# Performance work log

Measured on AMD Instinct MI355X. Metric: run time of the kernel, lower is better.

Reference implementation:

```python
import jax, jax.numpy as jnp
import numpy as np

N = 50000      # nodes
E = 800000     # edges
IN = 128       # in_channels
HID = 32       # hidden_channels per head
HEADS = 4
OUT = 16       # out_channels
NEG_SLOPE_ATT = 0.2   # GATv2Conv default negative_slope
NEG_SLOPE_ACT = 0.01  # F.leaky_relu default
EPS = 1e-16


def setup_inputs() -> dict:
    key = jax.random.key(0)
    ks = jax.random.split(key, 13)
    d1 = HEADS * HID  # 128
    g = lambda k, shape, fan: jax.random.normal(k, shape, jnp.float32) * (1.0 / np.sqrt(fan))
    return {
        "x": jax.random.normal(ks[0], (N, IN), jnp.float32),
        "edge_index": jax.random.randint(ks[1], (2, E), 0, N, dtype=jnp.int32),
        "edge_weight": jax.random.uniform(ks[2], (E,), jnp.float32),
        # conv1 (GATv2): lin_l, lin_r, att, bias
        "Wl1": g(ks[3], (IN, d1), IN), "Wr1": g(ks[4], (IN, d1), IN),
        "att1": g(ks[5], (HEADS, HID), HID), "b1": jnp.zeros((d1,), jnp.float32),
        # conv2
        "Wl2": g(ks[6], (d1, d1), d1), "Wr2": g(ks[7], (d1, d1), d1),
        "att2": g(ks[8], (HEADS, HID), HID), "b2": jnp.zeros((d1,), jnp.float32),
        # classifier
        "Wc": g(ks[9], (d1, OUT), d1), "bc": jnp.zeros((OUT,), jnp.float32),
    }


def gatv2_layer(x, Wl, Wr, att, bias, src, dst):
    n = x.shape[0]
    xl = (x @ Wl).reshape(n, HEADS, HID)  # source transform
    xr = (x @ Wr).reshape(n, HEADS, HID)  # target transform
    m = xl[src] + xr[dst]                                    # [Etot, H, C]
    e = jnp.sum(jax.nn.leaky_relu(m, NEG_SLOPE_ATT) * att, axis=-1)  # [Etot, H]
    # segment softmax over incoming edges of each target node
    emax = jax.ops.segment_max(e, dst, num_segments=n)       # [N, H]
    ex = jnp.exp(e - emax[dst])
    denom = jax.ops.segment_sum(ex, dst, num_segments=n)     # [N, H]
    alpha = ex / (denom[dst] + EPS)                          # [Etot, H]
    out = jax.ops.segment_sum(xl[src] * alpha[:, :, None], dst, num_segments=n)  # [N, H, C]
    return out.reshape(n, HEADS * HID) + bias


def reference(x, edge_index, edge_weight, Wl1, Wr1, att1, b1, Wl2, Wr2, att2, b2, Wc, bc):
    # GATv2Conv default add_self_loops=True
    loops = jnp.arange(N, dtype=edge_index.dtype)
    src = jnp.concatenate([edge_index[0], loops])
    dst = jnp.concatenate([edge_index[1], loops])
    h = gatv2_layer(x, Wl1, Wr1, att1, b1, src, dst)
    h = jax.nn.leaky_relu(h, NEG_SLOPE_ACT)
    h = gatv2_layer(h, Wl2, Wr2, att2, b2, src, dst)
    h = jax.nn.leaky_relu(h, NEG_SLOPE_ACT)
    logits = h @ Wc + bc
    return (logits, h)
```

## Files before the change

kernel.cpp:

```cpp
#include <hip/hip_runtime.h>
#include <hip/hip_fp16.h>


#define LOG2E 1.4426950408889634f
#define AST 40

typedef short bf16x8 __attribute__((ext_vector_type(8)));
typedef float f32x4 __attribute__((ext_vector_type(4)));

__device__ __forceinline__ unsigned short f2bf(float f) {
  union { float f; unsigned u; } x; x.f = f;
  unsigned r = x.u + 0x7fffu + ((x.u >> 16) & 1u);
  return (unsigned short)(r >> 16);
}
__device__ __forceinline__ float bf2f(unsigned short h) {
  union { unsigned u; float f; } x; x.u = ((unsigned)h) << 16;
  return x.f;
}
__device__ __forceinline__ void split4(float4 v, ushort4& h, ushort4& l) {
  h.x = f2bf(v.x); l.x = f2bf(v.x - bf2f(h.x));
  h.y = f2bf(v.y); l.y = f2bf(v.y - bf2f(h.y));
  h.z = f2bf(v.z); l.z = f2bf(v.z - bf2f(h.z));
  h.w = f2bf(v.w); l.w = f2bf(v.w - bf2f(h.w));
}

__device__ __forceinline__ float mixlo(float a, unsigned b, float c) {
  float d;
  asm("v_fma_mix_f32 %0, %1, %2, %3 op_sel_hi:[0,1,0]"
      : "=v"(d) : "v"(a), "v"(b), "v"(c));
  return d;
}
__device__ __forceinline__ float mixhi(float a, unsigned b, float c) {
  float d;
  asm("v_fma_mix_f32 %0, %1, %2, %3 op_sel:[0,1,0] op_sel_hi:[0,1,0]"
      : "=v"(d) : "v"(a), "v"(b), "v"(c));
  return d;
}
__device__ __forceinline__ float mixlo_abs(float a, unsigned b, float c) {
  float d;
  asm("v_fma_mix_f32 %0, %1, |%2|, %3 op_sel_hi:[0,1,0]"
      : "=v"(d) : "v"(a), "v"(b), "v"(c));
  return d;
}
__device__ __forceinline__ float mixhi_abs(float a, unsigned b, float c) {
  float d;
  asm("v_fma_mix_f32 %0, %1, |%2|, %3 op_sel:[0,1,0] op_sel_hi:[0,1,0]"
      : "=v"(d) : "v"(a), "v"(b), "v"(c));
  return d;
}
__device__ __forceinline__ unsigned pk_add(unsigned a, unsigned b) {
  union { unsigned u; __half2 h; } x, y, r;
  x.u = a; y.u = b;
  r.h = __hadd2(x.h, y.h);
  return r.u;
}


__global__ __launch_bounds__(256) void zero_i32(int* __restrict__ p, int n) {
  int i = blockIdx.x * 256 + threadIdx.x;
  if (i < n) p[i] = 0;
}

__global__ __launch_bounds__(256) void scan_blk(const int* __restrict__ cnt,
                                                int* __restrict__ excl,
                                                int* __restrict__ bsum, int n) {
  __shared__ int s[256];
  int t = threadIdx.x, i = blockIdx.x * 256 + t;
  int v = (i < n) ? (cnt[i] + 1) : 0;
  s[t] = v;
  __syncthreads();
#pragma unroll
  for (int off = 1; off < 256; off <<= 1) {
    int u = (t >= off) ? s[t - off] : 0;
    __syncthreads();
    s[t] += u;
    __syncthreads();
  }
  if (i < n) excl[i] = s[t] - v;
  if (t == 255) bsum[blockIdx.x] = s[255];
}

__global__ __launch_bounds__(256) void scan_bsum(int* __restrict__ bsum, int nb,
                                                 int* __restrict__ row_start, int n) {
  __shared__ int s[256];
  int t = threadIdx.x;
  int v = (t < nb) ? bsum[t] : 0;
  s[t] = v;
  __syncthreads();
#pragma unroll
  for (int off = 1; off < 256; off <<= 1) {
    int u = (t >= off) ? s[t - off] : 0;
    __syncthreads();
    s[t] += u;
    __syncthreads();
  }
  if (t < nb) bsum[t] = s[t] - v;
  if (t == 255) row_start[n] = s[255];
}

__global__ __launch_bounds__(256) void scan_add(int* __restrict__ row_start,
                                                const int* __restrict__ bsum,
                                                int* __restrict__ wpos,
                                                int* __restrict__ csr,
                                                int n, int padBase) {
  int i = blockIdx.x * 256 + threadIdx.x;
  if (i < n) {
    int r = row_start[i] + bsum[blockIdx.x];
    row_start[i] = r;
    wpos[i] = r + 1;
    csr[r] = i;
  }
  if (blockIdx.x == 0 && threadIdx.x < 16) csr[padBase + threadIdx.x] = 0;
}

__global__ __launch_bounds__(256) void convert_count(
    const float* __restrict__ Wl1, const float* __restrict__ Wr1,
    const float* __restrict__ Wl2, const float* __restrict__ Wr2,
    unsigned short* __restrict__ BT1h, unsigned short* __restrict__ BT1l,
    unsigned short* __restrict__ BT2h, unsigned short* __restrict__ BT2l,
    const int* __restrict__ dst, int* __restrict__ cnt, int E) {
  int b = blockIdx.x;
  if (b >= 256) {
    int i = (b - 256) * 256 + threadIdx.x;
    if (i < E) atomicAdd(&cnt[dst[i]], 1);
    return;
  }
  const float* Wl = (b < 128) ? Wl1 : Wl2;
  const float* Wr = (b < 128) ? Wr1 : Wr2;
  unsigned short* BTh = (b < 128) ? BT1h : BT2h;
  unsigned short* BTl = (b < 128) ? BT1l : BT2l;
  int idx = (b & 127) * 256 + threadIdx.x;
  int col = idx >> 7, k = idx & 127;
  float v = (col < 128) ? Wl[k * 128 + col] : Wr[k * 128 + (col - 128)];
  unsigned short h = f2bf(v);
  BTh[idx] = h;
  BTl[idx] = f2bf(v - bf2f(h));
}

enum { IN_F32 = 0, IN_BFPAIR = 1 };
template <int MODE, int FUSE>
__global__ __launch_bounds__(256) void gemm_mfma(
    const float* __restrict__ Af,
    const unsigned short* __restrict__ Ah, const unsigned short* __restrict__ Al,
    const unsigned short* __restrict__ BTh, const unsigned short* __restrict__ BTl,
    __half* __restrict__ Cl, __half* __restrict__ Cr, int nrows,
    const int* __restrict__ esrc, const int* __restrict__ edst,
    int* __restrict__ wpos, int* __restrict__ csr, int E, int sliceSize) {
  __shared__ __align__(16) unsigned short smem[4 * 128 * AST];
  int tid = threadIdx.x;
  int bx, by;
  if (FUSE) {
    int g = blockIdx.x / 9, r = blockIdx.x - g * 9;
    if (r < 5) {
      int sid = g * 5 + r;
      if (sid < 1024) {
        int per = (E + 1023) >> 10;
        int b0 = sid * per;
        int cnt = min(per, E - b0);
        if (cnt > 0) {
          int* ss = (int*)smem;
          int* sd = ss + per;
          for (int i = tid; i < cnt; i += 256) {
            ss[i] = esrc[b0 + i];
            sd[i] = edst[b0 + i];
          }
          __syncthreads();
          for (int sl = 0; sl < 8; ++sl) {
            int lo = sl * sliceSize, hi = lo + sliceSize;
            for (int i = tid; i < cnt; i += 256) {
              int d = sd[i];
              if (d >= lo && d < hi) {
                int p = atomicAdd(&wpos[d], 1);
                csr[p] = ss[i];
              }
            }
          }
        }
      }
      return;
    }
    int gid = g * 4 + (r - 5);
    int nbx = (nrows + 127) >> 7;
    if (gid >= nbx * 2) return;
    bx = gid >> 1;
    by = gid & 1;
  } else {
    bx = blockIdx.x;
    by = blockIdx.y;
  }

  unsigned short* sAh = smem;
  unsigned short* sAl = smem + 5120;
  unsigned short* sBh = smem + 10240;
  unsigned short* sBl = smem + 15360;

  int wave = tid >> 6, lane = tid & 63;
  int rowBase = bx * 128;
  int colBase = by * 128;
  int rowHalf = (wave >> 1) * 64;
  int colHalf = (wave & 1) * 64;
  int l15 = lane & 15, quad = lane >> 4;

  f32x4 acc[4][4];
#pragma unroll
  for (int m = 0; m < 4; ++m)
#pragma unroll
    for (int n = 0; n < 4; ++n) acc[m][n] = (f32x4){0.f, 0.f, 0.f, 0.f};

  for (int kc = 0; kc < 4; ++kc) {
#pragma unroll
    for (int i = 0; i < 2; ++i) {
      int idx = tid + i * 256;
      int row = idx >> 2, seg = idx & 3;
      int gr = rowBase + row;
      if (MODE == IN_F32) {
        float4 v0 = make_float4(0.f, 0.f, 0.f, 0.f), v1 = v0;
        if (gr < nrows) {
          v0 = *(const float4*)&Af[(size_t)gr * 128 + kc * 32 + seg * 8];
          v1 = *(const float4*)&Af[(size_t)gr * 128 + kc * 32 + seg * 8 + 4];
        }
        ushort4 h0, l0, h1, l1;
        split4(v0, h0, l0);
        split4(v1, h1, l1);
        *(ushort4*)&sAh[row * AST + seg * 8] = h0;
        *(ushort4*)&sAh[row * AST + seg * 8 + 4] = h1;
        *(ushort4*)&sAl[row * AST + seg * 8] = l0;
        *(ushort4*)&sAl[row * AST + seg * 8 + 4] = l1;
      } else {
        uint4 vh = make_uint4(0, 0, 0, 0), vl = vh;
        if (gr < nrows) {
          vh = *(const uint4*)&Ah[(size_t)gr * 128 + kc * 32 + seg * 8];
          vl = *(const uint4*)&Al[(size_t)gr * 128 + kc * 32 + seg * 8];
        }
        *(uint4*)&sAh[row * AST + seg * 8] = vh;
        *(uint4*)&sAl[row * AST + seg * 8] = vl;
      }
    }
#pragma unroll
    for (int i = 0; i < 2; ++i) {
      int idx = tid + i * 256;
      int col = idx >> 2, seg = idx & 3;
      *(uint4*)&sBh[col * AST + seg * 8] =
          *(const uint4*)&BTh[(size_t)(colBase + col) * 128 + kc * 32 + seg * 8];
      *(uint4*)&sBl[col * AST + seg * 8] =
          *(const uint4*)&BTl[(size_t)(colBase + col) * 128 + kc * 32 + seg * 8];
    }
    __syncthreads();

    bf16x8 afh[4], afl[4], bfh[4], bfl[4];
#pragma unroll
    for (int m = 0; m < 4; ++m) {
      int r = rowHalf + m * 16 + l15;
      afh[m] = *(const bf16x8*)&sAh[r * AST + quad * 8];
      afl[m] = *(const bf16x8*)&sAl[r * AST + quad * 8];
    }
#pragma unroll
    for (int n = 0; n < 4; ++n) {
      int cc = colHalf + n * 16 + l15;
      bfh[n] = *(const bf16x8*)&sBh[cc * AST + quad * 8];
      bfl[n] = *(const bf16x8*)&sBl[cc * AST + quad * 8];
    }
#pragma unroll
    for (int m = 0; m < 4; ++m)
#pragma unroll
      for (int n = 0; n < 4; ++n) {
        acc[m][n] = __builtin_amdgcn_mfma_f32_16x16x32_bf16(afh[m], bfh[n], acc[m][n], 0, 0, 0);
        acc[m][n] = __builtin_amdgcn_mfma_f32_16x16x32_bf16(afh[m], bfl[n], acc[m][n], 0, 0, 0);
        acc[m][n] = __builtin_amdgcn_mfma_f32_16x16x32_bf16(afl[m], bfh[n], acc[m][n], 0, 0, 0);
      }
    __syncthreads();
  }

  __half* __restrict__ C = (by == 0) ? Cl : Cr;
#pragma unroll
  for (int m = 0; m < 4; ++m)
#pragma unroll
    for (int r = 0; r < 4; ++r) {
      int grow = rowBase + rowHalf + m * 16 + quad * 4 + r;
      if (grow < nrows) {
#pragma unroll
        for (int n = 0; n < 4; ++n)
          C[(size_t)grow * 128 + colHalf + n * 16 + l15] = __float2half(acc[m][n][r]);
      }
    }
}

__global__ __launch_bounds__(256) void gat_attn(const __half* __restrict__ xl,
                                                const __half* __restrict__ xr,
                                                const int* __restrict__ row_start,
                                                const int* __restrict__ csr,
                                                const float* __restrict__ att,
                                                const float* __restrict__ bias,
                                                float* __restrict__ ofp,
                                                unsigned short* __restrict__ ohi,
                                                unsigned short* __restrict__ olo,
                                                int n_nodes) {
  int node = blockIdx.x * 4 + (threadIdx.x >> 6);
  if (node >= n_nodes) return;
  int lane = threadIdx.x & 63;
  int slot = lane >> 4;
  int l15 = lane & 15;
  int c0 = l15 * 8;

  unsigned hxr[4];
  {
    uint4 raw = *(const uint4*)&xr[(size_t)node * 128 + c0];
    const unsigned* q = (const unsigned*)&raw;
    hxr[0] = q[0]; hxr[1] = q[1]; hxr[2] = q[2]; hxr[3] = q[3];
  }
  float a06[8], a04[8];
  {
    float4 a0 = *(const float4*)&att[c0];
    float4 a1 = *(const float4*)&att[c0 + 4];
    float av[8] = {a0.x, a0.y, a0.z, a0.w, a1.x, a1.y, a1.z, a1.w};
    const float C06 = 0.6f * LOG2E, C04 = 0.4f * LOG2E;
#pragma unroll
    for (int k = 0; k < 8; ++k) { a06[k] = av[k] * C06; a04[k] = av[k] * C04; }
  }

  float acc[8];
#pragma unroll
  for (int k = 0; k < 8; ++k) acc[k] = 0.f;
  float lsum = 0.f;

#define EDGE_BODY(SRC, PVALID)                                                 \
  {                                                                            \
    uint4 raw = *(const uint4*)&xl[(size_t)(unsigned)(SRC)*128 + c0];          \
    const unsigned* xp = (const unsigned*)&raw;                                \
    float e0 = 0.f, e1 = 0.f;                                                  \
    _Pragma("unroll") for (int j = 0; j < 4; ++j) {                            \
      unsigned tw = pk_add(xp[j], hxr[j]);                                     \
      e0 = mixlo(a06[2 * j], tw, e0);                                          \
      e0 = mixlo_abs(a04[2 * j], tw, e0);                                      \
      e1 = mixhi(a06[2 * j + 1], tw, e1);                                      \
      e1 = mixhi_abs(a04[2 * j + 1], tw, e1);                                  \
    }                                                                          \
    float e = e0 + e1;                                                         \
    e += __shfl_xor(e, 1);                                                     \
    e += __shfl_xor(e, 2);                                                     \
    float p = (PVALID) ? __builtin_amdgcn_exp2f(e) : 0.f;                      \
    lsum += p;                                                                 \
    _Pragma("unroll") for (int j = 0; j < 4; ++j) {                            \
      acc[2 * j] = mixlo(p, xp[j], acc[2 * j]);                                \
      acc[2 * j + 1] = mixhi(p, xp[j], acc[2 * j + 1]);                        \
    }                                                                          \
  }

  int beg = row_start[node], end = row_start[node + 1];
  int deg = end - beg;
  int fullEnd = beg + (deg & ~15);

  for (int base = beg; base < fullEnd; base += 16) {
    int b0 = base + 4 * slot;
    int s0 = csr[b0], s1 = csr[b0 + 1], s2 = csr[b0 + 2], s3 = csr[b0 + 3];
    EDGE_BODY(s0, true);
    EDGE_BODY(s1, true);
    EDGE_BODY(s2, true);
    EDGE_BODY(s3, true);
  }
  for (int base = fullEnd; base < end; base += 4) {
    int idx = base + slot;
    int src = csr[idx];
    EDGE_BODY(src, idx < end);
  }
#undef EDGE_BODY

  lsum += __shfl_xor(lsum, 16);
  lsum += __shfl_xor(lsum, 32);
#pragma unroll
  for (int k = 0; k < 8; ++k) {
    acc[k] += __shfl_xor(acc[k], 16);
    acc[k] += __shfl_xor(acc[k], 32);
  }

  if (slot == 0) {
    float4 b0v = *(const float4*)&bias[c0];
    float4 b1v = *(const float4*)&bias[c0 + 4];
    float bv[8] = {b0v.x, b0v.y, b0v.z, b0v.w, b1v.x, b1v.y, b1v.z, b1v.w};
    float inv = 1.f / (lsum + 1e-16f);
    float o[8];
#pragma unroll
    for (int k = 0; k < 8; ++k) {
      float v = fmaf(acc[k], inv, bv[k]);
      o[k] = fmaf(0.495f, fabsf(v), 0.505f * v);
    }
    if (ofp) {
      *(float4*)&ofp[(size_t)node * 128 + c0] = make_float4(o[0], o[1], o[2], o[3]);
      *(float4*)&ofp[(size_t)node * 128 + c0 + 4] = make_float4(o[4], o[5], o[6], o[7]);
    }
    if (ohi) {
      ushort4 h0, h1, lo0, lo1;
      h0.x = f2bf(o[0]); lo0.x = f2bf(o[0] - bf2f(h0.x));
      h0.y = f2bf(o[1]); lo0.y = f2bf(o[1] - bf2f(h0.y));
      h0.z = f2bf(o[2]); lo0.z = f2bf(o[2] - bf2f(h0.z));
      h0.w = f2bf(o[3]); lo0.w = f2bf(o[3] - bf2f(h0.w));
      h1.x = f2bf(o[4]); lo1.x = f2bf(o[4] - bf2f(h1.x));
      h1.y = f2bf(o[5]); lo1.y = f2bf(o[5] - bf2f(h1.y));
      h1.z = f2bf(o[6]); lo1.z = f2bf(o[6] - bf2f(h1.z));
      h1.w = f2bf(o[7]); lo1.w = f2bf(o[7] - bf2f(h1.w));
      *(ushort4*)&ohi[(size_t)node * 128 + c0] = h0;
      *(ushort4*)&ohi[(size_t)node * 128 + c0 + 4] = h1;
      *(ushort4*)&olo[(size_t)node * 128 + c0] = lo0;
      *(ushort4*)&olo[(size_t)node * 128 + c0 + 4] = lo1;
    }
  }
}

__global__ __launch_bounds__(256) void classifier_kernel(const float4* __restrict__ h4,
                                                         const float* __restrict__ Wc,
                                                         const float* __restrict__ bc,
                                                         float* __restrict__ logits,
                                                         int n) {
  __shared__ float sW[2048];
  __shared__ float sb[16];
  int t = threadIdx.x;
#pragma unroll
  for (int i = 0; i < 8; ++i) sW[t + i * 256] = Wc[t + i * 256];
  if (t < 16) sb[t] = bc[t];
  __syncthreads();
  int node = blockIdx.x * 256 + t;
  if (node >= n) return;
  float acc[16];
#pragma unroll
  for (int o = 0; o < 16; ++o) acc[o] = sb[o];
  for (int c4 = 0; c4 < 32; ++c4) {
    float4 hv = h4[(unsigned)node * 32 + c4];
    const float* w = &sW[c4 * 64];
#pragma unroll
    for (int o = 0; o < 16; ++o) {
      acc[o] = fmaf(hv.x, w[o], acc[o]);
      acc[o] = fmaf(hv.y, w[16 + o], acc[o]);
      acc[o] = fmaf(hv.z, w[32 + o], acc[o]);
      acc[o] = fmaf(hv.w, w[48 + o], acc[o]);
    }
  }
#pragma unroll
  for (int q = 0; q < 4; ++q)
    *(float4*)&logits[(size_t)node * 16 + q * 4] =
        make_float4(acc[q * 4], acc[q * 4 + 1], acc[q * 4 + 2], acc[q * 4 + 3]);
}


extern "C" void kernel_launch(void* const* d_in, const int* in_sizes, int n_in,
                              void* d_out, int out_size, void* d_ws, size_t ws_size,
                              hipStream_t stream) {
  const float* x    = (const float*)d_in[0];
  const int*   ei   = (const int*)d_in[1];
  const float* Wl1  = (const float*)d_in[3];
  const float* Wr1  = (const float*)d_in[4];
  const float* att1 = (const float*)d_in[5];
  const float* b1   = (const float*)d_in[6];
  const float* Wl2  = (const float*)d_in[7];
  const float* Wr2  = (const float*)d_in[8];
  const float* att2 = (const float*)d_in[9];
  const float* b2   = (const float*)d_in[10];
  const float* Wc   = (const float*)d_in[11];
  const float* bc   = (const float*)d_in[12];

  const int N = in_sizes[0] / 128;
  const int E = in_sizes[1] / 2;

  float* outp   = (float*)d_out;
  float* logits = outp;
  float* hout   = outp + (size_t)N * 16;
  unsigned short* h1h = (unsigned short*)hout;
  unsigned short* h1l = h1h + (size_t)N * 128;

  char* ws = (char*)d_ws;
  __half* xlbuf = (__half*)ws;                ws += (size_t)N * 128 * 2;
  __half* xrbuf = (__half*)ws;                ws += (size_t)N * 128 * 2;
  unsigned short* WT1h = (unsigned short*)ws; ws += 256 * 128 * 2;
  unsigned short* WT1l = (unsigned short*)ws; ws += 256 * 128 * 2;
  unsigned short* WT2h = (unsigned short*)ws; ws += 256 * 128 * 2;
  unsigned short* WT2l = (unsigned short*)ws; ws += 256 * 128 * 2;
  int* cnt       = (int*)ws;                  ws += (size_t)N * 4;
  int* row_start = (int*)ws;                  ws += (size_t)(N + 1) * 4;
  int* wpos      = (int*)ws;                  ws += (size_t)N * 4;
  int* bsum      = (int*)ws;                  ws += 256 * 4;
  int* csr       = (int*)ws;                  ws += (size_t)(E + N + 16) * 4;

  const int* esrc = ei;
  const int* edst = ei + E;

  int gN = (N + 255) / 256, gE = (E + 255) / 256;
  int gAttn = (N + 3) / 4;
  int sliceSize = (N + 7) / 8;

  int nbx = (N + 127) / 128;
  int nGemm = nbx * 2;
  int groups = (1024 + 4) / 5;
  int g2 = (nGemm + 3) / 4;
  if (g2 > groups) groups = g2;
  int gFused = groups * 9;

  zero_i32<<<gN, 256, 0, stream>>>(cnt, N);
  convert_count<<<256 + gE, 256, 0, stream>>>(Wl1, Wr1, Wl2, Wr2,
                                              WT1h, WT1l, WT2h, WT2l,
                                              edst, cnt, E);
  scan_blk<<<gN, 256, 0, stream>>>(cnt, row_start, bsum, N);
  scan_bsum<<<1, 256, 0, stream>>>(bsum, gN, row_start, N);
  scan_add<<<gN, 256, 0, stream>>>(row_start, bsum, wpos, csr, N, E + N);

  gemm_mfma<IN_F32, 1><<<gFused, 256, 0, stream>>>(
      x, nullptr, nullptr, WT1h, WT1l, xlbuf, xrbuf, N,
      esrc, edst, wpos, csr, E, sliceSize);
  gat_attn<<<gAttn, 256, 0, stream>>>(xlbuf, xrbuf, row_start, csr, att1, b1,
                                      nullptr, h1h, h1l, N);

  gemm_mfma<IN_BFPAIR, 0><<<dim3(nbx, 2), 256, 0, stream>>>(
      nullptr, h1h, h1l, WT2h, WT2l, xlbuf, xrbuf, N,
      nullptr, nullptr, nullptr, nullptr, 0, 0);
  gat_attn<<<gAttn, 256, 0, stream>>>(xlbuf, xrbuf, row_start, csr, att2, b2,
                                      hout, nullptr, nullptr, N);

  classifier_kernel<<<(N + 255) / 256, 256, 0, stream>>>((const float4*)hout, Wc, bc,
                                                         logits, N);
}
```

Baseline: 319.4 us.

## Fuse classifier into attention, store layer-1 output as fp16, rework CSR scatter

Folds the classifier matmul into the second attention kernel so the separate classifier launch and its re-read of h go away. The layer-1 activation is now stored as a single fp16 array instead of a bf16 hi/lo pair, halving that intermediate traffic, and the GEMM splits it back into bf16 pairs on load. This trades some precision, since fp16 carries fewer mantissa bits than the bf16 pair. The CSR scatter is reorganized so each block handles one chunk-slice pair and streams edges directly instead of staging them in shared memory. It also adds nontemporal loads, restructures the edge loop so four gathers are issued before compute, and raises wave priority around the MFMAs.

```diff
diff --git a/kernel.cpp b/kernel.cpp
--- a/kernel.cpp
+++ b/kernel.cpp
@@ -53,6 +53,29 @@
   x.u = a; y.u = b;
   r.h = __hadd2(x.h, y.h);
   return r.u;
+}
+
+__device__ __forceinline__ float edot(uint4 raw, const unsigned* hxr,
+                                      const float* a06, const float* a04) {
+  const unsigned* xp = (const unsigned*)&raw;
+  float ea = 0.f, eb = 0.f;
+#pragma unroll
+  for (int j = 0; j < 4; ++j) {
+    unsigned tw = pk_add(xp[j], hxr[j]);
+    ea = mixlo(a06[2 * j], tw, ea);
+    ea = mixlo_abs(a04[2 * j], tw, ea);
+    eb = mixhi(a06[2 * j + 1], tw, eb);
+    eb = mixhi_abs(a04[2 * j + 1], tw, eb);
+  }
+  return ea + eb;
+}
+__device__ __forceinline__ void accupd(float p, uint4 raw, float* acc) {
+  const unsigned* xp = (const unsigned*)&raw;
+#pragma unroll
+  for (int j = 0; j < 4; ++j) {
+    acc[2 * j] = mixlo(p, xp[j], acc[2 * j]);
+    acc[2 * j + 1] = mixhi(p, xp[j], acc[2 * j + 1]);
+  }
 }
 
 
@@ -122,7 +145,7 @@
   int b = blockIdx.x;
   if (b >= 256) {
     int i = (b - 256) * 256 + threadIdx.x;
-    if (i < E) atomicAdd(&cnt[dst[i]], 1);
+    if (i < E) atomicAdd(&cnt[__builtin_nontemporal_load(&dst[i])], 1);
     return;
   }
   const float* Wl = (b < 128) ? Wl1 : Wl2;
@@ -137,11 +160,12 @@
   BTl[idx] = f2bf(v - bf2f(h));
 }
 
-enum { IN_F32 = 0, IN_BFPAIR = 1 };
+enum { IN_F32 = 0, IN_F16 = 1 };
+#define NSCAT 1152
+#define NCHUNK 128
 template <int MODE, int FUSE>
 __global__ __launch_bounds__(256) void gemm_mfma(
-    const float* __restrict__ Af,
-    const unsigned short* __restrict__ Ah, const unsigned short* __restrict__ Al,
+    const float* __restrict__ Af, const __half* __restrict__ Af16,
     const unsigned short* __restrict__ BTh, const unsigned short* __restrict__ BTl,
     __half* __restrict__ Cl, __half* __restrict__ Cr, int nrows,
     const int* __restrict__ esrc, const int* __restrict__ edst,
@@ -153,26 +177,22 @@
     int g = blockIdx.x / 9, r = blockIdx.x - g * 9;
     if (r < 5) {
       int sid = g * 5 + r;
-      if (sid < 1024) {
-        int per = (E + 1023) >> 10;
-        int b0 = sid * per;
-        int cnt = min(per, E - b0);
-        if (cnt > 0) {
-          int* ss = (int*)smem;
-          int* sd = ss + per;
-          for (int i = tid; i < cnt; i += 256) {
-            ss[i] = esrc[b0 + i];
-            sd[i] = edst[b0 + i];
-          }
-          __syncthreads();
-          for (int sl = 0; sl < 8; ++sl) {
-            int lo = sl * sliceSize, hi = lo + sliceSize;
-            for (int i = tid; i < cnt; i += 256) {
-              int d = sd[i];
-              if (d >= lo && d < hi) {
-                int p = atomicAdd(&wpos[d], 1);
-                csr[p] = ss[i];
-              }
+      if (sid < NSCAT) {
+        int slice = blockIdx.x & 7;
+        int chunk = (g >> 3) * 5;
+        for (int gp = g & ~7; gp < g; ++gp)
+          chunk += (((slice - gp) & 7) < 5) ? 1 : 0;
+        if (chunk < NCHUNK) {
+          int per = (E + NCHUNK - 1) / NCHUNK;
+          int b0 = chunk * per;
+          int ee = min(b0 + per, E);
+          int lo = slice * sliceSize, hi = lo + sliceSize;
+          for (int i = b0 + tid; i < ee; i += 256) {
+            int d = __builtin_nontemporal_load(&edst[i]);
+            if (d >= lo && d < hi) {
+              int s = __builtin_nontemporal_load(&esrc[i]);
+              int p = atomicAdd(&wpos[d], 1);
+              csr[p] = s;
             }
           }
         }
@@ -213,28 +233,29 @@
       int idx = tid + i * 256;
       int row = idx >> 2, seg = idx & 3;
       int gr = rowBase + row;
+      float4 v0 = make_float4(0.f, 0.f, 0.f, 0.f), v1 = v0;
       if (MODE == IN_F32) {
-        float4 v0 = make_float4(0.f, 0.f, 0.f, 0.f), v1 = v0;
         if (gr < nrows) {
           v0 = *(const float4*)&Af[(size_t)gr * 128 + kc * 32 + seg * 8];
           v1 = *(const float4*)&Af[(size_t)gr * 128 + kc * 32 + seg * 8 + 4];
         }
-        ushort4 h0, l0, h1, l1;
-        split4(v0, h0, l0);
-        split4(v1, h1, l1);
-        *(ushort4*)&sAh[row * AST + seg * 8] = h0;
-        *(ushort4*)&sAh[row * AST + seg * 8 + 4] = h1;
-        *(ushort4*)&sAl[row * AST + seg * 8] = l0;
-        *(ushort4*)&sAl[row * AST + seg * 8 + 4] = l1;
       } else {
-        uint4 vh = make_uint4(0, 0, 0, 0), vl = vh;
         if (gr < nrows) {
-          vh = *(const uint4*)&Ah[(size_t)gr * 128 + kc * 32 + seg * 8];
-          vl = *(const uint4*)&Al[(size_t)gr * 128 + kc * 32 + seg * 8];
+          uint4 raw = *(const uint4*)&Af16[(size_t)gr * 128 + kc * 32 + seg * 8];
+          const __half* hp = (const __half*)&raw;
+          v0 = make_float4(__half2float(hp[0]), __half2float(hp[1]),
+                           __half2float(hp[2]), __half2float(hp[3]));
+          v1 = make_float4(__half2float(hp[4]), __half2float(hp[5]),
+                           __half2float(hp[6]), __half2float(hp[7]));
         }
-        *(uint4*)&sAh[row * AST + seg * 8] = vh;
-        *(uint4*)&sAl[row * AST + seg * 8] = vl;
       }
+      ushort4 h0, l0, h1, l1;
+      split4(v0, h0, l0);
+      split4(v1, h1, l1);
+      *(ushort4*)&sAh[row * AST + seg * 8] = h0;
+      *(ushort4*)&sAh[row * AST + seg * 8 + 4] = h1;
+      *(ushort4*)&sAl[row * AST + seg * 8] = l0;
+      *(ushort4*)&sAl[row * AST + seg * 8 + 4] = l1;
     }
 #pragma unroll
     for (int i = 0; i < 2; ++i) {
@@ -260,6 +281,7 @@
       bfh[n] = *(const bf16x8*)&sBh[cc * AST + quad * 8];
       bfl[n] = *(const bf16x8*)&sBl[cc * AST + quad * 8];
     }
+    __builtin_amdgcn_s_setprio(1);
 #pragma unroll
     for (int m = 0; m < 4; ++m)
 #pragma unroll
@@ -268,6 +290,7 @@
         acc[m][n] = __builtin_amdgcn_mfma_f32_16x16x32_bf16(afh[m], bfl[n], acc[m][n], 0, 0, 0);
         acc[m][n] = __builtin_amdgcn_mfma_f32_16x16x32_bf16(afl[m], bfh[n], acc[m][n], 0, 0, 0);
       }
+    __builtin_amdgcn_s_setprio(0);
     __syncthreads();
   }
 
@@ -292,12 +315,21 @@
                                                 const float* __restrict__ att,
                                                 const float* __restrict__ bias,
                                                 float* __restrict__ ofp,
-                                                unsigned short* __restrict__ ohi,
-                                                unsigned short* __restrict__ olo,
+                                                __half* __restrict__ oh16,
+                                                const float* __restrict__ Wc,
+                                                const float* __restrict__ bc,
+                                                float* __restrict__ logits,
                                                 int n_nodes) {
-  int node = blockIdx.x * 4 + (threadIdx.x >> 6);
+  __shared__ float sW[2048];
+  int tid = threadIdx.x;
+  if (logits) {
+#pragma unroll
+    for (int i = 0; i < 8; ++i) sW[tid + i * 256] = Wc[tid + i * 256];
+    __syncthreads();
+  }
+  int node = blockIdx.x * 4 + (tid >> 6);
   if (node >= n_nodes) return;
-  int lane = threadIdx.x & 63;
+  int lane = tid & 63;
   int slot = lane >> 4;
   int l15 = lane & 15;
   int c0 = l15 * 8;
@@ -323,47 +355,49 @@
   for (int k = 0; k < 8; ++k) acc[k] = 0.f;
   float lsum = 0.f;
 
-#define EDGE_BODY(SRC, PVALID)                                                 \
-  {                                                                            \
-    uint4 raw = *(const uint4*)&xl[(size_t)(unsigned)(SRC)*128 + c0];          \
-    const unsigned* xp = (const unsigned*)&raw;                                \
-    float e0 = 0.f, e1 = 0.f;                                                  \
-    _Pragma("unroll") for (int j = 0; j < 4; ++j) {                            \
-      unsigned tw = pk_add(xp[j], hxr[j]);                                     \
-      e0 = mixlo(a06[2 * j], tw, e0);                                          \
-      e0 = mixlo_abs(a04[2 * j], tw, e0);                                      \
-      e1 = mixhi(a06[2 * j + 1], tw, e1);                                      \
-      e1 = mixhi_abs(a04[2 * j + 1], tw, e1);                                  \
-    }                                                                          \
-    float e = e0 + e1;                                                         \
-    e += __shfl_xor(e, 1);                                                     \
-    e += __shfl_xor(e, 2);                                                     \
-    float p = (PVALID) ? __builtin_amdgcn_exp2f(e) : 0.f;                      \
-    lsum += p;                                                                 \
-    _Pragma("unroll") for (int j = 0; j < 4; ++j) {                            \
-      acc[2 * j] = mixlo(p, xp[j], acc[2 * j]);                                \
-      acc[2 * j + 1] = mixhi(p, xp[j], acc[2 * j + 1]);                        \
-    }                                                                          \
-  }
-
   int beg = row_start[node], end = row_start[node + 1];
   int deg = end - beg;
   int fullEnd = beg + (deg & ~15);
 
   for (int base = beg; base < fullEnd; base += 16) {
     int b0 = base + 4 * slot;
-    int s0 = csr[b0], s1 = csr[b0 + 1], s2 = csr[b0 + 2], s3 = csr[b0 + 3];
-    EDGE_BODY(s0, true);
-    EDGE_BODY(s1, true);
-    EDGE_BODY(s2, true);
-    EDGE_BODY(s3, true);
+    int s0 = __builtin_nontemporal_load(&csr[b0]);
+    int s1 = __builtin_nontemporal_load(&csr[b0 + 1]);
+    int s2 = __builtin_nontemporal_load(&csr[b0 + 2]);
+    int s3 = __builtin_nontemporal_load(&csr[b0 + 3]);
+    uint4 r0 = *(const uint4*)&xl[(size_t)(unsigned)s0 * 128 + c0];
+    uint4 r1 = *(const uint4*)&xl[(size_t)(unsigned)s1 * 128 + c0];
+    uint4 r2 = *(const uint4*)&xl[(size_t)(unsigned)s2 * 128 + c0];
+    uint4 r3 = *(const uint4*)&xl[(size_t)(unsigned)s3 * 128 + c0];
+    float e0 = edot(r0, hxr, a06, a04);
+    float e1 = edot(r1, hxr, a06, a04);
+    float e2 = edot(r2, hxr, a06, a04);
+    float e3 = edot(r3, hxr, a06, a04);
+    e0 += __shfl_xor(e0, 1); e1 += __shfl_xor(e1, 1);
+    e2 += __shfl_xor(e2, 1); e3 += __shfl_xor(e3, 1);
+    e0 += __shfl_xor(e0, 2); e1 += __shfl_xor(e1, 2);
+    e2 += __shfl_xor(e2, 2); e3 += __shfl_xor(e3, 2);
+    float p0 = __builtin_amdgcn_exp2f(e0);
+    float p1 = __builtin_amdgcn_exp2f(e1);
+    float p2 = __builtin_amdgcn_exp2f(e2);
+    float p3 = __builtin_amdgcn_exp2f(e3);
+    lsum += (p0 + p1) + (p2 + p3);
+    accupd(p0, r0, acc);
+    accupd(p1, r1, acc);
+    accupd(p2, r2, acc);
+    accupd(p3, r3, acc);
   }
   for (int base = fullEnd; base < end; base += 4) {
     int idx = base + slot;
-    int src = csr[idx];
-    EDGE_BODY(src, idx < end);
-  }
-#undef EDGE_BODY
+    int src = __builtin_nontemporal_load(&csr[idx]);
+    uint4 raw = *(const uint4*)&xl[(size_t)(unsigned)src * 128 + c0];
+    float e = edot(raw, hxr, a06, a04);
+    e += __shfl_xor(e, 1);
+    e += __shfl_xor(e, 2);
+    float p = (idx < end) ? __builtin_amdgcn_exp2f(e) : 0.f;
+    lsum += p;
+    accupd(p, raw, acc);
+  }
 
   lsum += __shfl_xor(lsum, 16);
   lsum += __shfl_xor(lsum, 32);
@@ -373,71 +407,62 @@
     acc[k] += __shfl_xor(acc[k], 32);
   }
 
-  if (slot == 0) {
+  float o[8];
+  {
     float4 b0v = *(const float4*)&bias[c0];
     float4 b1v = *(const float4*)&bias[c0 + 4];
     float bv[8] = {b0v.x, b0v.y, b0v.z, b0v.w, b1v.x, b1v.y, b1v.z, b1v.w};
     float inv = 1.f / (lsum + 1e-16f);
-    float o[8];
 #pragma unroll
     for (int k = 0; k < 8; ++k) {
       float v = fmaf(acc[k], inv, bv[k]);
       o[k] = fmaf(0.495f, fabsf(v), 0.505f * v);
     }
+  }
+
+  if (slot == 0) {
     if (ofp) {
       *(float4*)&ofp[(size_t)node * 128 + c0] = make_float4(o[0], o[1], o[2], o[3]);
       *(float4*)&ofp[(size_t)node * 128 + c0 + 4] = make_float4(o[4], o[5], o[6], o[7]);
     }
-    if (ohi) {
-      ushort4 h0, h1, lo0, lo1;
-      h0.x = f2bf(o[0]); lo0.x = f2bf(o[0] - bf2f(h0.x));
-      h0.y = f2bf(o[1]); lo0.y = f2bf(o[1] - bf2f(h0.y));
-      h0.z = f2bf(o[2]); lo0.z = f2bf(o[2] - bf2f(h0.z));
-      h0.w = f2bf(o[3]); lo0.w = f2bf(o[3] - bf2f(h0.w));
-      h1.x = f2bf(o[4]); lo1.x = f2bf(o[4] - bf2f(h1.x));
-      h1.y = f2bf(o[5]); lo1.y = f2bf(o[5] - bf2f(h1.y));
-      h1.z = f2bf(o[6]); lo1.z = f2bf(o[6] - bf2f(h1.z));
-      h1.w = f2bf(o[7]); lo1.w = f2bf(o[7] - bf2f(h1.w));
-      *(ushort4*)&ohi[(size_t)node * 128 + c0] = h0;
-      *(ushort4*)&ohi[(size_t)node * 128 + c0 + 4] = h1;
-      *(ushort4*)&olo[(size_t)node * 128 + c0] = lo0;
-      *(ushort4*)&olo[(size_t)node * 128 + c0 + 4] = lo1;
-    }
-  }
-}
-
-__global__ __launch_bounds__(256) void classifier_kernel(const float4* __restrict__ h4,
-                                                         const float* __restrict__ Wc,
-                                                         const float* __restrict__ bc,
-                                                         float* __restrict__ logits,
-                                                         int n) {
-  __shared__ float sW[2048];
-  __shared__ float sb[16];
-  int t = threadIdx.x;
-#pragma unroll
-  for (int i = 0; i < 8; ++i) sW[t + i * 256] = Wc[t + i * 256];
-  if (t < 16) sb[t] = bc[t];
-  __syncthreads();
-  int node = blockIdx.x * 256 + t;
-  if (node >= n) return;
-  float acc[16];
-#pragma unroll
-  for (int o = 0; o < 16; ++o) acc[o] = sb[o];
-  for (int c4 = 0; c4 < 32; ++c4) {
-    float4 hv = h4[(unsigned)node * 32 + c4];
-    const float* w = &sW[c4 * 64];
-#pragma unroll
-    for (int o = 0; o < 16; ++o) {
-      acc[o] = fmaf(hv.x, w[o], acc[o]);
-      acc[o] = fmaf(hv.y, w[16 + o], acc[o]);
-      acc[o] = fmaf(hv.z, w[32 + o], acc[o]);
-      acc[o] = fmaf(hv.w, w[48 + o], acc[o]);
-    }
-  }
-#pragma unroll
-  for (int q = 0; q < 4; ++q)
-    *(float4*)&logits[(size_t)node * 16 + q * 4] =
-        make_float4(acc[q * 4], acc[q * 4 + 1], acc[q * 4 + 2], acc[q * 4 + 3]);
+    if (oh16) {
+      ushort4 ha, hb;
+      ha.x = __half_as_ushort(__float2half(o[0]));
+      ha.y = __half_as_ushort(__float2half(o[1]));
+      ha.z = __half_as_ushort(__float2half(o[2]));
+      ha.w = __half_as_ushort(__float2half(o[3]));
+      hb.x = __half_as_ushort(__float2half(o[4]));
+      hb.y = __half_as_ushort(__float2half(o[5]));
+      hb.z = __half_as_ushort(__float2half(o[6]));
+      hb.w = __half_as_ushort(__float2half(o[7]));
+      *(ushort4*)&oh16[(size_t)node * 128 + c0] = ha;
+      *(ushort4*)&oh16[(size_t)node * 128 + c0 + 4] = hb;
+    }
+  }
+
+  if (logits) {
+    int ob = slot * 4;
+    float pj0 = 0.f, pj1 = 0.f, pj2 = 0.f, pj3 = 0.f;
+#pragma unroll
+    for (int k = 0; k < 8; ++k) {
+      float4 w = *(const float4*)&sW[(c0 + k) * 16 + ob];
+      pj0 = fmaf(o[k], w.x, pj0);
+      pj1 = fmaf(o[k], w.y, pj1);
+      pj2 = fmaf(o[k], w.z, pj2);
+      pj3 = fmaf(o[k], w.w, pj3);
+    }
+#pragma unroll
+    for (int m = 1; m < 16; m <<= 1) {
+      pj0 += __shfl_xor(pj0, m);
+      pj1 += __shfl_xor(pj1, m);
+      pj2 += __shfl_xor(pj2, m);
+      pj3 += __shfl_xor(pj3, m);
+    }
+    if (l15 < 4) {
+      float pv = (l15 == 0) ? pj0 : (l15 == 1) ? pj1 : (l15 == 2) ? pj2 : pj3;
+      logits[(size_t)node * 16 + ob + l15] = pv + bc[ob + l15];
+    }
+  }
 }
 
 
@@ -463,8 +488,7 @@
   float* outp   = (float*)d_out;
   float* logits = outp;
   float* hout   = outp + (size_t)N * 16;
-  unsigned short* h1h = (unsigned short*)hout;
-  unsigned short* h1l = h1h + (size_t)N * 128;
+  __half* h1f16 = (__half*)hout;
 
   char* ws = (char*)d_ws;
   __half* xlbuf = (__half*)ws;                ws += (size_t)N * 128 * 2;
@@ -488,7 +512,7 @@
 
   int nbx = (N + 127) / 128;
   int nGemm = nbx * 2;
-  int groups = (1024 + 4) / 5;
+  int groups = (NSCAT + 4) / 5;
   int g2 = (nGemm + 3) / 4;
   if (g2 > groups) groups = g2;
   int gFused = groups * 9;
@@ -502,17 +526,14 @@
   scan_add<<<gN, 256, 0, stream>>>(row_start, bsum, wpos, csr, N, E + N);
 
   gemm_mfma<IN_F32, 1><<<gFused, 256, 0, stream>>>(
-      x, nullptr, nullptr, WT1h, WT1l, xlbuf, xrbuf, N,
+      x, nullptr, WT1h, WT1l, xlbuf, xrbuf, N,
       esrc, edst, wpos, csr, E, sliceSize);
   gat_attn<<<gAttn, 256, 0, stream>>>(xlbuf, xrbuf, row_start, csr, att1, b1,
-                                      nullptr, h1h, h1l, N);
-
-  gemm_mfma<IN_BFPAIR, 0><<<dim3(nbx, 2), 256, 0, stream>>>(
-      nullptr, h1h, h1l, WT2h, WT2l, xlbuf, xrbuf, N,
+                                      nullptr, h1f16, nullptr, nullptr, nullptr, N);
+
+  gemm_mfma<IN_F16, 0><<<dim3(nbx, 2), 256, 0, stream>>>(
+      nullptr, h1f16, WT2h, WT2l, xlbuf, xrbuf, N,
       nullptr, nullptr, nullptr, nullptr, 0, 0);
   gat_attn<<<gAttn, 256, 0, stream>>>(xlbuf, xrbuf, row_start, csr, att2, b2,
-                                      hout, nullptr, nullptr, N);
-
-  classifier_kernel<<<(N + 255) / 256, 256, 0, stream>>>((const float4*)hout, Wc, bc,
-                                                         logits, N);
-}
+                                      hout, nullptr, Wc, bc, logits, N);
+}
```

Result: slower. 363.0 us (+13.6%).
